# Performance work log

Hardware: AMD Instinct MI355X
Metric: run time of the kernel (lower is better)

Reference implementation:

```python
import jax, jax.numpy as jnp
import numpy as np

B, T, E, H = 2, 2048, 768, 12
D = E // H  # head_dim = 64
EPS = 1e-5


def layer_norm(x, scale, shift):
    mean = x.mean(axis=-1, keepdims=True)
    # torch .var() default is unbiased (ddof=1)
    var = x.var(axis=-1, keepdims=True, ddof=1)
    return scale * (x - mean) / jnp.sqrt(var + EPS) + shift


def gelu(x):
    c = jnp.sqrt(jnp.asarray(2.0 / jnp.pi, dtype=x.dtype))
    return 0.5 * x * (1.0 + jnp.tanh(c * (x + 0.044715 * x * x * x)))


def setup_inputs() -> dict:
    key = jax.random.key(0)
    ks = jax.random.split(key, 12)
    s = 0.02
    return {
        "x": jax.random.normal(ks[0], (B, T, E), jnp.float32),
        "wq": jax.random.normal(ks[1], (E, E), jnp.float32) * s,
        "wk": jax.random.normal(ks[2], (E, E), jnp.float32) * s,
        "wv": jax.random.normal(ks[3], (E, E), jnp.float32) * s,
        "wo": jax.random.normal(ks[4], (E, E), jnp.float32) * s,
        "bo": jnp.zeros((E,), jnp.float32),
        "ln1_scale": jnp.ones((E,), jnp.float32),
        "ln1_shift": jnp.zeros((E,), jnp.float32),
        "ln2_scale": jnp.ones((E,), jnp.float32),
        "ln2_shift": jnp.zeros((E,), jnp.float32),
        "w1": jax.random.normal(ks[5], (E, 4 * E), jnp.float32) * s,
        "b1": jnp.zeros((4 * E,), jnp.float32),
        "w2": jax.random.normal(ks[6], (4 * E, E), jnp.float32) * s,
        "b2": jnp.zeros((E,), jnp.float32),
    }


def reference(x, wq, wk, wv, wo, bo, ln1_scale, ln1_shift, ln2_scale, ln2_shift,
              w1, b1, w2, b2):
    b, t, e = x.shape
    resid = x
    h = layer_norm(x, ln1_scale, ln1_shift)
    # qkv projections (no bias), split heads -> [b, H, t, D]
    q = (h @ wq).reshape(b, t, H, D).transpose(0, 2, 1, 3)
    k = (h @ wk).reshape(b, t, H, D).transpose(0, 2, 1, 3)
    v = (h @ wv).reshape(b, t, H, D).transpose(0, 2, 1, 3)
    scores = jnp.einsum("bhqd,bhkd->bhqk", q, k) / jnp.sqrt(jnp.asarray(D, x.dtype))
    causal = jnp.tril(jnp.ones((t, t), bool))
    scores = jnp.where(causal[None, None], scores, -jnp.inf)
    attn = jax.nn.softmax(scores, axis=-1)  # dropout p=0 (eval)
    ctx = jnp.einsum("bhqk,bhkd->bhqd", attn, v)
    ctx = ctx.transpose(0, 2, 1, 3).reshape(b, t, e)
    h = ctx @ wo + bo
    x = h + resid

    resid = x
    h = layer_norm(x, ln2_scale, ln2_shift)
    h = gelu(h @ w1 + b1) @ w2 + b2
    return h + resid
```

## Files before the change

kernel.cpp:

```cpp
#include <hip/hip_runtime.h>
#include <hip/hip_bf16.h>
#include <math.h>

typedef __bf16 bf16_t;
typedef __bf16 bf16x4 __attribute__((ext_vector_type(4)));
typedef __bf16 bf16x8 __attribute__((ext_vector_type(8)));
typedef float f32x4 __attribute__((ext_vector_type(4)));

#define TB 2048
#define BB 2
#define EE 768
#define HH 12
#define MM (BB * TB)
#define E3 (3 * EE)
#define E4 (4 * EE)

#define GLL16(g, l)                                                        \
  __builtin_amdgcn_global_load_lds(                                       \
      (const __attribute__((address_space(1))) void*)(g),                 \
      (__attribute__((address_space(3))) void*)(l), 16, 0, 0)

__global__ __launch_bounds__(256) void k_transpose_all(
    const float* __restrict__ wq, const float* __restrict__ wk,
    const float* __restrict__ wv, const float* __restrict__ wo,
    const float* __restrict__ w1, const float* __restrict__ w2,
    bf16_t* __restrict__ wqkvT, bf16_t* __restrict__ woT,
    bf16_t* __restrict__ w1T, bf16_t* __restrict__ w2T) {
  __shared__ bf16_t tile[64][72];
  int id = blockIdx.x;
  const float* src;
  bf16_t* dst;
  int K, N, kt, nt;
  if (id < 576) {
    int m = id / 144, t = id - m * 144;
    kt = (t / 12) * 64; nt = (t % 12) * 64; K = 768; N = 768;
    src = (m == 0) ? wq : (m == 1) ? wk : (m == 2) ? wv : wo;
    dst = (m < 3) ? wqkvT + (size_t)m * 768 * 768 : woT;
  } else if (id < 1152) {
    int t = id - 576;
    kt = (t / 48) * 64; nt = (t % 48) * 64; K = 768; N = 3072;
    src = w1; dst = w1T;
  } else {
    int t = id - 1152;
    kt = (t / 12) * 64; nt = (t % 12) * 64; K = 3072; N = 768;
    src = w2; dst = w2T;
  }
  int tid = threadIdx.x;
  int r = tid >> 2, c = (tid & 3) * 16;
  const float* s = src + (size_t)(kt + r) * N + nt + c;
  bf16x8 t0, t1;
#pragma unroll
  for (int j = 0; j < 8; j++) { t0[j] = (bf16_t)s[j]; t1[j] = (bf16_t)s[8 + j]; }
  *(bf16x8*)&tile[r][c] = t0;
  *(bf16x8*)&tile[r][c + 8] = t1;
  __syncthreads();
  bf16_t* d = dst + (size_t)(nt + r) * K + kt + c;
  bf16x8 o0, o1;
#pragma unroll
  for (int j = 0; j < 8; j++) { o0[j] = tile[c + j][r]; o1[j] = tile[c + 8 + j][r]; }
  *(bf16x8*)d = o0;
  *(bf16x8*)(d + 8) = o1;
}

__global__ __launch_bounds__(256) void k_transpose_v(const bf16_t* __restrict__ qkv,
                                                     bf16_t* __restrict__ vt) {
  __shared__ bf16_t tile[64][72];
  int tt = blockIdx.x;
  int bh = blockIdx.y;
  int b = bh / HH, h = bh - b * HH;
  int tid = threadIdx.x;
  int r = tid >> 2, c = (tid & 3) * 16;
  const bf16_t* src = qkv + (size_t)(b * TB + tt * 64 + r) * E3 + 2 * EE + h * 64 + c;
  *(bf16x8*)&tile[r][c] = *(const bf16x8*)src;
  *(bf16x8*)&tile[r][c + 8] = *(const bf16x8*)(src + 8);
  __syncthreads();
  bf16_t* dst = vt + ((size_t)bh * 64 + r) * TB + tt * 64 + c;
  bf16x8 o0, o1;
#pragma unroll
  for (int j = 0; j < 8; j++) { o0[j] = tile[c + j][r]; o1[j] = tile[c + 8 + j][r]; }
  *(bf16x8*)dst = o0;
  *(bf16x8*)(dst + 8) = o1;
}

__global__ __launch_bounds__(256) void k_layernorm_bf16(
    const float* __restrict__ x, const float* __restrict__ sc,
    const float* __restrict__ sh, bf16_t* __restrict__ out) {
  int wave = threadIdx.x >> 6, lane = threadIdx.x & 63;
  int row = blockIdx.x * 4 + wave;
  const float* xr = x + (size_t)row * EE;
  float v[12];
  float s = 0.f, sq = 0.f;
#pragma unroll
  for (int i = 0; i < 12; i++) {
    float t = xr[lane + 64 * i];
    v[i] = t; s += t; sq += t * t;
  }
#pragma unroll
  for (int off = 1; off < 64; off <<= 1) {
    s += __shfl_xor(s, off);
    sq += __shfl_xor(sq, off);
  }
  float mean = s * (1.f / EE);
  float var = (sq - (float)EE * mean * mean) * (1.f / (EE - 1));
  float rstd = rsqrtf(var + 1e-5f);
  bf16_t* orow = out + (size_t)row * EE;
#pragma unroll
  for (int i = 0; i < 12; i++) {
    int e = lane + 64 * i;
    orow[e] = (bf16_t)(sc[e] * (v[i] - mean) * rstd + sh[e]);
  }
}

__global__ __launch_bounds__(256) void k_gemm128(
    const bf16_t* __restrict__ A, const bf16_t* __restrict__ Bt,
    int M, int N, int K, int kLen, int epi,
    float* __restrict__ outf, bf16_t* __restrict__ outb,
    const float* __restrict__ bias, const float* __restrict__ resid) {
  __shared__ bf16_t As[128 * 64];
  __shared__ bf16_t Bs[128 * 64];
  int tid = threadIdx.x;
  int wave = tid >> 6, lane = tid & 63;
  int m0 = blockIdx.y * 128, n0 = blockIdx.x * 128;
  int kOff = blockIdx.z * kLen;
  int wm = (wave >> 1) * 64, wn = (wave & 1) * 64;
  int lm = lane & 15, quad = lane >> 4;

  int srow = wave * 32 + (lane >> 3);
  int scol = (((lane & 7) ^ ((lane >> 3) & 7)) * 8);
  const bf16_t* Ap = A + (size_t)(m0 + srow) * K + kOff + scol;
  const bf16_t* Bp = Bt + (size_t)(n0 + srow) * K + kOff + scol;
  bf16_t* ldsA[4];
  bf16_t* ldsB[4];
#pragma unroll
  for (int j = 0; j < 4; j++) {
    ldsA[j] = &As[(wave * 32 + j * 8) * 64];
    ldsB[j] = &Bs[(wave * 32 + j * 8) * 64];
  }

  f32x4 acc[4][4];
#pragma unroll
  for (int i = 0; i < 4; i++)
#pragma unroll
    for (int j = 0; j < 4; j++) acc[i][j] = (f32x4){0.f, 0.f, 0.f, 0.f};

  for (int k0 = 0; k0 < kLen; k0 += 64) {
    __syncthreads();
#pragma unroll
    for (int j = 0; j < 4; j++) {
      GLL16(Ap + k0 + (size_t)j * 8 * K, ldsA[j]);
      GLL16(Bp + k0 + (size_t)j * 8 * K, ldsB[j]);
    }
    __syncthreads();
#pragma unroll
    for (int c = 0; c < 2; c++) {
      bf16x8 af[4], bfr[4];
#pragma unroll
      for (int i = 0; i < 4; i++) {
        int r = wm + i * 16 + lm;
        af[i] = *(const bf16x8*)&As[r * 64 + (((c * 4 + quad) ^ (lm & 7)) * 8)];
      }
#pragma unroll
      for (int j = 0; j < 4; j++) {
        int r = wn + j * 16 + lm;
        bfr[j] = *(const bf16x8*)&Bs[r * 64 + (((c * 4 + quad) ^ (lm & 7)) * 8)];
      }
#pragma unroll
      for (int i = 0; i < 4; i++)
#pragma unroll
        for (int j = 0; j < 4; j++)
          acc[i][j] = __builtin_amdgcn_mfma_f32_16x16x32_bf16(af[i], bfr[j], acc[i][j], 0, 0, 0);
    }
  }

  size_t pbase = (size_t)blockIdx.z * M * N;
#pragma unroll
  for (int i = 0; i < 4; i++) {
#pragma unroll
    for (int j = 0; j < 4; j++) {
      int col = n0 + wn + j * 16 + lm;
#pragma unroll
      for (int r = 0; r < 4; r++) {
        int row = m0 + wm + i * 16 + quad * 4 + r;
        size_t o = (size_t)row * N + col;
        float c = acc[i][j][r];
        if (epi == 0) {
          outb[o] = (bf16_t)c;
        } else if (epi == 1) {
          float xg = c + bias[col];
          float u2 = xg * 1.5957691216057308f + xg * xg * xg * 0.07135481627561393f;
          float t = 1.f - 2.f / (__expf(u2) + 1.f);
          outb[o] = (bf16_t)(0.5f * xg * (1.f + t));
        } else if (epi == 2) {
          outf[o] = c + bias[col] + resid[o];
        } else {
          outb[pbase + o] = (bf16_t)c;
        }
      }
    }
  }
}

__global__ __launch_bounds__(256) void k_reduce_ln2(
    const bf16_t* __restrict__ p, const float* __restrict__ bo_,
    const float* __restrict__ x, const float* __restrict__ sc,
    const float* __restrict__ sh, float* __restrict__ x1,
    bf16_t* __restrict__ h2) {
  int wave = threadIdx.x >> 6, lane = threadIdx.x & 63;
  int row = blockIdx.x * 4 + wave;
  const bf16_t* p0 = p + (size_t)row * EE;
  const bf16_t* p1 = p + (size_t)(MM + row) * EE;
  const float* xr = x + (size_t)row * EE;
  float v[12];
  float s = 0.f, sq = 0.f;
#pragma unroll
  for (int i = 0; i < 12; i++) {
    int e = lane + 64 * i;
    float t = (float)p0[e] + (float)p1[e] + bo_[e] + xr[e];
    v[i] = t; s += t; sq += t * t;
  }
#pragma unroll
  for (int off = 1; off < 64; off <<= 1) {
    s += __shfl_xor(s, off);
    sq += __shfl_xor(sq, off);
  }
  float mean = s * (1.f / EE);
  float var = (sq - (float)EE * mean * mean) * (1.f / (EE - 1));
  float rstd = rsqrtf(var + 1e-5f);
  float* x1r = x1 + (size_t)row * EE;
  bf16_t* h2r = h2 + (size_t)row * EE;
#pragma unroll
  for (int i = 0; i < 12; i++) {
    int e = lane + 64 * i;
    x1r[e] = v[i];
    h2r[e] = (bf16_t)(sc[e] * (v[i] - mean) * rstd + sh[e]);
  }
}

__global__ __launch_bounds__(256) void k_reduce_out(
    const bf16_t* __restrict__ p, const float* __restrict__ b2,
    const float* __restrict__ x1, float* __restrict__ out) {
  size_t e = ((size_t)blockIdx.x * 256 + threadIdx.x) * 8;
  bf16x8 a0 = *(const bf16x8*)(p + e);
  bf16x8 a1 = *(const bf16x8*)(p + (size_t)MM * EE + e);
  bf16x8 a2 = *(const bf16x8*)(p + (size_t)2 * MM * EE + e);
  bf16x8 a3 = *(const bf16x8*)(p + (size_t)3 * MM * EE + e);
  int col = (int)(e % EE);
#pragma unroll
  for (int j = 0; j < 8; j++) {
    out[e + j] = (float)a0[j] + (float)a1[j] + (float)a2[j] + (float)a3[j] +
                 b2[col + j] + x1[e + j];
  }
}

__global__ __launch_bounds__(256) void k_attn_mfma(const bf16_t* __restrict__ qkv,
                                                   const bf16_t* __restrict__ vt,
                                                   bf16_t* __restrict__ opart,
                                                   float* __restrict__ lpart) {
  __shared__ bf16_t Qs[64][72];
  __shared__ bf16_t Ks[64][72];
  __shared__ bf16_t Vt[64][72];
  __shared__ bf16_t Ps[4][16][72];

  int bh = blockIdx.x;
  int y = blockIdx.y;
  int qt, c, nsplit;
  if (y < 32)      { qt = 24 + (y >> 2); c = y & 3; nsplit = 4; }
  else if (y < 56) { int z = y - 32; qt = 16 + z / 3; c = z - (z / 3) * 3; nsplit = 3; }
  else if (y < 72) { int z = y - 56; qt = 8 + (z >> 1); c = z & 1; nsplit = 2; }
  else             { qt = y - 72; c = 0; nsplit = 1; }
  int ntiles = qt + 1;
  int len = (ntiles + nsplit - 1) / nsplit;
  int k0t = c * len;
  int k1t = k0t + len < ntiles ? k0t + len : ntiles;

  int b = bh / HH, h = bh - b * HH;
  int q0 = qt * 64;
  int tid = threadIdx.x;
  int wave = tid >> 6, lane = tid & 63;
  int lm = lane & 15, quad = lane >> 4;
  int sr = tid >> 2, sc = (tid & 3) * 16;
  const bf16_t* vt_bh = vt + (size_t)bh * 64 * TB;

  {
    const bf16_t* src = qkv + (size_t)(b * TB + q0 + sr) * E3 + h * 64 + sc;
    bf16x8 u0 = *(const bf16x8*)src;
    bf16x8 u1 = *(const bf16x8*)(src + 8);
    bf16x8 s0, s1;
#pragma unroll
    for (int j = 0; j < 8; j++) {
      s0[j] = (bf16_t)((float)u0[j] * 0.125f);
      s1[j] = (bf16_t)((float)u1[j] * 0.125f);
    }
    *(bf16x8*)(&Qs[sr][sc]) = s0;
    *(bf16x8*)(&Qs[sr][sc + 8]) = s1;
  }
  __syncthreads();
  bf16x8 qf0 = *(const bf16x8*)(&Qs[wave * 16 + lm][quad * 8]);
  bf16x8 qf1 = *(const bf16x8*)(&Qs[wave * 16 + lm][32 + quad * 8]);

  f32x4 o_acc[4];
#pragma unroll
  for (int nt = 0; nt < 4; nt++) o_acc[nt] = (f32x4){0.f, 0.f, 0.f, 0.f};
  float l = 0.f;

  for (int kt = k0t; kt < k1t; kt++) {
    __syncthreads();
    {
      const bf16_t* ksrc = qkv + (size_t)(b * TB + kt * 64 + sr) * E3 + EE + h * 64 + sc;
      *(bf16x8*)(&Ks[sr][sc]) = *(const bf16x8*)ksrc;
      *(bf16x8*)(&Ks[sr][sc + 8]) = *(const bf16x8*)(ksrc + 8);
      const bf16_t* vsrc = vt_bh + (size_t)sr * TB + kt * 64 + sc;
      *(bf16x8*)(&Vt[sr][sc]) = *(const bf16x8*)vsrc;
      *(bf16x8*)(&Vt[sr][sc + 8]) = *(const bf16x8*)(vsrc + 8);
    }
    __syncthreads();

    f32x4 st[4];
#pragma unroll
    for (int nt = 0; nt < 4; nt++) {
      st[nt] = (f32x4){0.f, 0.f, 0.f, 0.f};
      bf16x8 kf0 = *(const bf16x8*)(&Ks[nt * 16 + lm][quad * 8]);
      bf16x8 kf1 = *(const bf16x8*)(&Ks[nt * 16 + lm][32 + quad * 8]);
      st[nt] = __builtin_amdgcn_mfma_f32_16x16x32_bf16(kf0, qf0, st[nt], 0, 0, 0);
      st[nt] = __builtin_amdgcn_mfma_f32_16x16x32_bf16(kf1, qf1, st[nt], 0, 0, 0);
    }
    if (kt == qt) {
#pragma unroll
      for (int nt = 0; nt < 4; nt++)
#pragma unroll
        for (int r = 0; r < 4; r++)
          if (nt * 16 + quad * 4 + r > wave * 16 + lm) st[nt][r] = -1e30f;
    }

#pragma unroll
    for (int nt = 0; nt < 4; nt++) {
      bf16x4 pk;
#pragma unroll
      for (int r = 0; r < 4; r++) {
        float p = __expf(st[nt][r]);
        pk[r] = (bf16_t)p;
        l += p;
      }
      *(bf16x4*)(&Ps[wave][lm][nt * 16 + quad * 4]) = pk;
    }

    bf16x8 pf0 = *(const bf16x8*)(&Ps[wave][lm][quad * 8]);
    bf16x8 pf1 = *(const bf16x8*)(&Ps[wave][lm][32 + quad * 8]);
#pragma unroll
    for (int nt = 0; nt < 4; nt++) {
      bf16x8 vf0 = *(const bf16x8*)(&Vt[nt * 16 + lm][quad * 8]);
      bf16x8 vf1 = *(const bf16x8*)(&Vt[nt * 16 + lm][32 + quad * 8]);
      o_acc[nt] = __builtin_amdgcn_mfma_f32_16x16x32_bf16(pf0, vf0, o_acc[nt], 0, 0, 0);
      o_acc[nt] = __builtin_amdgcn_mfma_f32_16x16x32_bf16(pf1, vf1, o_acc[nt], 0, 0, 0);
    }
  }

  l += __shfl_xor(l, 16);
  l += __shfl_xor(l, 32);
  size_t slot = (size_t)(bh * 32 + qt) * 4 + c;
  if (quad == 0) lpart[slot * 64 + wave * 16 + lm] = l;
  bf16_t* ob = opart + slot * 4096;
#pragma unroll
  for (int nt = 0; nt < 4; nt++)
#pragma unroll
    for (int r = 0; r < 4; r++)
      ob[(wave * 16 + quad * 4 + r) * 64 + nt * 16 + lm] = (bf16_t)o_acc[nt][r];
}

__global__ __launch_bounds__(256) void k_attn_reduce(
    const bf16_t* __restrict__ opart, const float* __restrict__ lpart,
    bf16_t* __restrict__ ctx) {
  int bh = blockIdx.x, qt = blockIdx.y;
  int b = bh / HH, h = bh - b * HH;
  int nsplit = qt >= 24 ? 4 : qt >= 16 ? 3 : qt >= 8 ? 2 : 1;
  int tid = threadIdx.x;
  int q = tid >> 2, dc = (tid & 3) * 16;
  size_t slot0 = (size_t)(bh * 32 + qt) * 4;
  float o[16];
#pragma unroll
  for (int j = 0; j < 16; j++) o[j] = 0.f;
  float lsum = 0.f;
  for (int c = 0; c < nsplit; c++) {
    const bf16_t* p = opart + (slot0 + c) * 4096 + q * 64 + dc;
    bf16x8 u0 = *(const bf16x8*)p;
    bf16x8 u1 = *(const bf16x8*)(p + 8);
#pragma unroll
    for (int j = 0; j < 8; j++) { o[j] += (float)u0[j]; o[8 + j] += (float)u1[j]; }
    lsum += lpart[(slot0 + c) * 64 + q];
  }
  float inv = 1.f / lsum;
  bf16_t* dst = ctx + (size_t)(b * TB + qt * 64 + q) * EE + h * 64 + dc;
  bf16x8 d0, d1;
#pragma unroll
  for (int j = 0; j < 8; j++) { d0[j] = (bf16_t)(o[j] * inv); d1[j] = (bf16_t)(o[8 + j] * inv); }
  *(bf16x8*)dst = d0;
  *(bf16x8*)(dst + 8) = d1;
}

extern "C" void kernel_launch(void* const* d_in, const int* in_sizes, int n_in,
                              void* d_out, int out_size, void* d_ws, size_t ws_size,
                              hipStream_t stream) {
  const float* x    = (const float*)d_in[0];
  const float* wq   = (const float*)d_in[1];
  const float* wk   = (const float*)d_in[2];
  const float* wv   = (const float*)d_in[3];
  const float* wo   = (const float*)d_in[4];
  const float* bo   = (const float*)d_in[5];
  const float* ln1s = (const float*)d_in[6];
  const float* ln1b = (const float*)d_in[7];
  const float* ln2s = (const float*)d_in[8];
  const float* ln2b = (const float*)d_in[9];
  const float* w1   = (const float*)d_in[10];
  const float* b1   = (const float*)d_in[11];
  const float* w2   = (const float*)d_in[12];
  const float* b2   = (const float*)d_in[13];
  float* out = (float*)d_out;

  char* ws = (char*)d_ws;
  size_t off = 0;
  auto alloc = [&](size_t bytes) {
    char* p = ws + off;
    off += (bytes + 255) & ~(size_t)255;
    return p;
  };
  float*  x1    = (float*) alloc((size_t)MM * EE * 4);
  bf16_t* w1T   = (bf16_t*)alloc((size_t)E4 * EE * 2);
  bf16_t* w2T   = (bf16_t*)alloc((size_t)EE * E4 * 2);
  bf16_t* woT   = (bf16_t*)alloc((size_t)EE * EE * 2);
  bf16_t* wqkvT = (bf16_t*)alloc((size_t)E3 * EE * 2);
  bf16_t* hbf   = (bf16_t*)alloc((size_t)MM * EE * 2);
  bf16_t* h2    = (bf16_t*)alloc((size_t)MM * EE * 2);
  bf16_t* vtb   = (bf16_t*)alloc((size_t)BB * HH * 64 * TB * 2);
  bf16_t* part  = (bf16_t*)alloc((size_t)4 * MM * EE * 2);
  bf16_t* opart = (bf16_t*)alloc((size_t)BB * HH * 32 * 4 * 4096 * 2);
  float*  lpart = (float*) alloc((size_t)BB * HH * 32 * 4 * 64 * 4);
  bf16_t* qkv   = (bf16_t*)alloc((size_t)MM * E3 * 2);
  bf16_t* hmid  = qkv;

  k_transpose_all<<<1728, 256, 0, stream>>>(wq, wk, wv, wo, w1, w2,
                                            wqkvT, woT, w1T, w2T);
  k_layernorm_bf16<<<MM / 4, 256, 0, stream>>>(x, ln1s, ln1b, hbf);
  k_gemm128<<<dim3(E3 / 128, MM / 128), 256, 0, stream>>>(hbf, wqkvT, MM, E3, EE, EE, 0,
                                                          nullptr, qkv, nullptr, nullptr);
  k_transpose_v<<<dim3(TB / 64, BB * HH), 256, 0, stream>>>(qkv, vtb);
  k_attn_mfma<<<dim3(BB * HH, 80), 256, 0, stream>>>(qkv, vtb, opart, lpart);
  k_attn_reduce<<<dim3(BB * HH, TB / 64), 256, 0, stream>>>(opart, lpart, hbf);
  k_gemm128<<<dim3(EE / 128, MM / 128, 2), 256, 0, stream>>>(hbf, woT, MM, EE, EE, 384, 3,
                                                             nullptr, part, nullptr, nullptr);
  k_reduce_ln2<<<MM / 4, 256, 0, stream>>>(part, bo, x, ln2s, ln2b, x1, h2);
  k_gemm128<<<dim3(E4 / 128, MM / 128), 256, 0, stream>>>(h2, w1T, MM, E4, EE, EE, 1,
                                                          nullptr, hmid, b1, nullptr);
  k_gemm128<<<dim3(EE / 128, MM / 128, 4), 256, 0, stream>>>(hmid, w2T, MM, EE, E4, E4 / 4, 3,
                                                             nullptr, part, nullptr, nullptr);
  k_reduce_out<<<(MM * EE / 8 + 255) / 256, 256, 0, stream>>>(part, b2, x1, out);
}
```

Measured before the change: 288.1 us.

## Double-buffer GEMM LDS tiles with K=32 steps and split-K 4 for out-projection

The 128x128 GEMM now uses two LDS buffers of K=32 and prefetches the next tile with global_load_lds while MFMAs run on the current one. This replaces the two barriers per K=64 step and is meant to overlap global-to-LDS transfer with compute. The XOR swizzle is dropped, which risks LDS bank conflicts on the fragment reads. The out-projection split-K goes from 2 to 4 with the LN2 reduce summing four partials, trading extra partial traffic for more blocks.

```diff
diff --git a/kernel.cpp b/kernel.cpp
--- a/kernel.cpp
+++ b/kernel.cpp
@@ -116,8 +116,8 @@
     int M, int N, int K, int kLen, int epi,
     float* __restrict__ outf, bf16_t* __restrict__ outb,
     const float* __restrict__ bias, const float* __restrict__ resid) {
-  __shared__ bf16_t As[128 * 64];
-  __shared__ bf16_t Bs[128 * 64];
+  __shared__ bf16_t As[2][128 * 32];
+  __shared__ bf16_t Bs[2][128 * 32];
   int tid = threadIdx.x;
   int wave = tid >> 6, lane = tid & 63;
   int m0 = blockIdx.y * 128, n0 = blockIdx.x * 128;
@@ -125,17 +125,12 @@
   int wm = (wave >> 1) * 64, wn = (wave & 1) * 64;
   int lm = lane & 15, quad = lane >> 4;
 
-  int srow = wave * 32 + (lane >> 3);
-  int scol = (((lane & 7) ^ ((lane >> 3) & 7)) * 8);
-  const bf16_t* Ap = A + (size_t)(m0 + srow) * K + kOff + scol;
-  const bf16_t* Bp = Bt + (size_t)(n0 + srow) * K + kOff + scol;
-  bf16_t* ldsA[4];
-  bf16_t* ldsB[4];
-#pragma unroll
-  for (int j = 0; j < 4; j++) {
-    ldsA[j] = &As[(wave * 32 + j * 8) * 64];
-    ldsB[j] = &Bs[(wave * 32 + j * 8) * 64];
-  }
+  int srow = wave * 32 + (lane >> 2);
+  int scol = (lane & 3) * 8;
+  const bf16_t* Ap0 = A + (size_t)(m0 + srow) * K + kOff + scol;
+  const bf16_t* Ap1 = A + (size_t)(m0 + srow + 16) * K + kOff + scol;
+  const bf16_t* Bp0 = Bt + (size_t)(n0 + srow) * K + kOff + scol;
+  const bf16_t* Bp1 = Bt + (size_t)(n0 + srow + 16) * K + kOff + scol;
 
   f32x4 acc[4][4];
 #pragma unroll
@@ -143,33 +138,35 @@
 #pragma unroll
     for (int j = 0; j < 4; j++) acc[i][j] = (f32x4){0.f, 0.f, 0.f, 0.f};
 
-  for (int k0 = 0; k0 < kLen; k0 += 64) {
+  int nIter = kLen >> 5;
+  GLL16(Ap0, &As[0][(wave * 32) * 32]);
+  GLL16(Ap1, &As[0][(wave * 32 + 16) * 32]);
+  GLL16(Bp0, &Bs[0][(wave * 32) * 32]);
+  GLL16(Bp1, &Bs[0][(wave * 32 + 16) * 32]);
+
+  for (int k = 0; k < nIter; k++) {
     __syncthreads();
-#pragma unroll
-    for (int j = 0; j < 4; j++) {
-      GLL16(Ap + k0 + (size_t)j * 8 * K, ldsA[j]);
-      GLL16(Bp + k0 + (size_t)j * 8 * K, ldsB[j]);
-    }
-    __syncthreads();
-#pragma unroll
-    for (int c = 0; c < 2; c++) {
-      bf16x8 af[4], bfr[4];
-#pragma unroll
-      for (int i = 0; i < 4; i++) {
-        int r = wm + i * 16 + lm;
-        af[i] = *(const bf16x8*)&As[r * 64 + (((c * 4 + quad) ^ (lm & 7)) * 8)];
-      }
-#pragma unroll
-      for (int j = 0; j < 4; j++) {
-        int r = wn + j * 16 + lm;
-        bfr[j] = *(const bf16x8*)&Bs[r * 64 + (((c * 4 + quad) ^ (lm & 7)) * 8)];
-      }
-#pragma unroll
-      for (int i = 0; i < 4; i++)
-#pragma unroll
-        for (int j = 0; j < 4; j++)
-          acc[i][j] = __builtin_amdgcn_mfma_f32_16x16x32_bf16(af[i], bfr[j], acc[i][j], 0, 0, 0);
-    }
+    int buf = k & 1;
+    if (k + 1 < nIter) {
+      int nb = buf ^ 1;
+      int ko = (k + 1) << 5;
+      GLL16(Ap0 + ko, &As[nb][(wave * 32) * 32]);
+      GLL16(Ap1 + ko, &As[nb][(wave * 32 + 16) * 32]);
+      GLL16(Bp0 + ko, &Bs[nb][(wave * 32) * 32]);
+      GLL16(Bp1 + ko, &Bs[nb][(wave * 32 + 16) * 32]);
+    }
+    bf16x8 af[4], bfr[4];
+#pragma unroll
+    for (int i = 0; i < 4; i++)
+      af[i] = *(const bf16x8*)&As[buf][(wm + i * 16 + lm) * 32 + quad * 8];
+#pragma unroll
+    for (int j = 0; j < 4; j++)
+      bfr[j] = *(const bf16x8*)&Bs[buf][(wn + j * 16 + lm) * 32 + quad * 8];
+#pragma unroll
+    for (int i = 0; i < 4; i++)
+#pragma unroll
+      for (int j = 0; j < 4; j++)
+        acc[i][j] = __builtin_amdgcn_mfma_f32_16x16x32_bf16(af[i], bfr[j], acc[i][j], 0, 0, 0);
   }
 
   size_t pbase = (size_t)blockIdx.z * M * N;
@@ -208,14 +205,17 @@
   int wave = threadIdx.x >> 6, lane = threadIdx.x & 63;
   int row = blockIdx.x * 4 + wave;
   const bf16_t* p0 = p + (size_t)row * EE;
-  const bf16_t* p1 = p + (size_t)(MM + row) * EE;
+  const bf16_t* p1 = p0 + (size_t)MM * EE;
+  const bf16_t* p2 = p0 + (size_t)2 * MM * EE;
+  const bf16_t* p3 = p0 + (size_t)3 * MM * EE;
   const float* xr = x + (size_t)row * EE;
   float v[12];
   float s = 0.f, sq = 0.f;
 #pragma unroll
   for (int i = 0; i < 12; i++) {
     int e = lane + 64 * i;
-    float t = (float)p0[e] + (float)p1[e] + bo_[e] + xr[e];
+    float t = (float)p0[e] + (float)p1[e] + (float)p2[e] + (float)p3[e] +
+              bo_[e] + xr[e];
     v[i] = t; s += t; sq += t * t;
   }
 #pragma unroll
@@ -445,7 +445,7 @@
   k_transpose_v<<<dim3(TB / 64, BB * HH), 256, 0, stream>>>(qkv, vtb);
   k_attn_mfma<<<dim3(BB * HH, 80), 256, 0, stream>>>(qkv, vtb, opart, lpart);
   k_attn_reduce<<<dim3(BB * HH, TB / 64), 256, 0, stream>>>(opart, lpart, hbf);
-  k_gemm128<<<dim3(EE / 128, MM / 128, 2), 256, 0, stream>>>(hbf, woT, MM, EE, EE, 384, 3,
+  k_gemm128<<<dim3(EE / 128, MM / 128, 4), 256, 0, stream>>>(hbf, woT, MM, EE, EE, 192, 3,
                                                              nullptr, part, nullptr, nullptr);
   k_reduce_ln2<<<MM / 4, 256, 0, stream>>>(part, bo, x, ln2s, ln2b, x1, h2);
   k_gemm128<<<dim3(E4 / 128, MM / 128), 256, 0, stream>>>(h2, w1T, MM, E4, EE, EE, 1,
```

After: 300.5 us. +4.3%, slower.

## Fuse LN1 into weight prep, write V transposed from QKV GEMM, prescale Wq

Applied to the files above, without the earlier changes.

Merges the LayerNorm-1 kernel into the weight transpose/convert kernel as extra blocks, removing one launch. The QKV GEMM epilogue now writes V tiles directly in transposed per-head layout, which removes the separate V transpose kernel and its read/write pass. The 1/sqrt(D) scale is folded into Wq during conversion, so the attention kernel loads Q without rescaling. This changes bf16 rounding of Q slightly, and the transposed V stores are 4-element strided writes.

```diff
diff --git a/kernel.cpp b/kernel.cpp
--- a/kernel.cpp
+++ b/kernel.cpp
@@ -20,22 +20,54 @@
       (const __attribute__((address_space(1))) void*)(g),                 \
       (__attribute__((address_space(3))) void*)(l), 16, 0, 0)
 
-__global__ __launch_bounds__(256) void k_transpose_all(
+__global__ __launch_bounds__(256) void k_prep(
     const float* __restrict__ wq, const float* __restrict__ wk,
     const float* __restrict__ wv, const float* __restrict__ wo,
     const float* __restrict__ w1, const float* __restrict__ w2,
     bf16_t* __restrict__ wqkvT, bf16_t* __restrict__ woT,
-    bf16_t* __restrict__ w1T, bf16_t* __restrict__ w2T) {
+    bf16_t* __restrict__ w1T, bf16_t* __restrict__ w2T,
+    const float* __restrict__ x, const float* __restrict__ ln1s,
+    const float* __restrict__ ln1b, bf16_t* __restrict__ hbf) {
   __shared__ bf16_t tile[64][72];
   int id = blockIdx.x;
+  int tid = threadIdx.x;
+  if (id >= 1728) {
+    int wave = tid >> 6, lane = tid & 63;
+    int row = (id - 1728) * 4 + wave;
+    const float* xr = x + (size_t)row * EE;
+    float v[12];
+    float s = 0.f, sq = 0.f;
+#pragma unroll
+    for (int i = 0; i < 12; i++) {
+      float t = xr[lane + 64 * i];
+      v[i] = t; s += t; sq += t * t;
+    }
+#pragma unroll
+    for (int off = 1; off < 64; off <<= 1) {
+      s += __shfl_xor(s, off);
+      sq += __shfl_xor(sq, off);
+    }
+    float mean = s * (1.f / EE);
+    float var = (sq - (float)EE * mean * mean) * (1.f / (EE - 1));
+    float rstd = rsqrtf(var + 1e-5f);
+    bf16_t* orow = hbf + (size_t)row * EE;
+#pragma unroll
+    for (int i = 0; i < 12; i++) {
+      int e = lane + 64 * i;
+      orow[e] = (bf16_t)(ln1s[e] * (v[i] - mean) * rstd + ln1b[e]);
+    }
+    return;
+  }
   const float* src;
   bf16_t* dst;
   int K, N, kt, nt;
+  float scl = 1.f;
   if (id < 576) {
     int m = id / 144, t = id - m * 144;
     kt = (t / 12) * 64; nt = (t % 12) * 64; K = 768; N = 768;
     src = (m == 0) ? wq : (m == 1) ? wk : (m == 2) ? wv : wo;
     dst = (m < 3) ? wqkvT + (size_t)m * 768 * 768 : woT;
+    if (m == 0) scl = 0.125f;
   } else if (id < 1152) {
     int t = id - 576;
     kt = (t / 48) * 64; nt = (t % 48) * 64; K = 768; N = 3072;
@@ -45,12 +77,14 @@
     kt = (t / 12) * 64; nt = (t % 12) * 64; K = 3072; N = 768;
     src = w2; dst = w2T;
   }
-  int tid = threadIdx.x;
   int r = tid >> 2, c = (tid & 3) * 16;
   const float* s = src + (size_t)(kt + r) * N + nt + c;
   bf16x8 t0, t1;
 #pragma unroll
-  for (int j = 0; j < 8; j++) { t0[j] = (bf16_t)s[j]; t1[j] = (bf16_t)s[8 + j]; }
+  for (int j = 0; j < 8; j++) {
+    t0[j] = (bf16_t)(s[j] * scl);
+    t1[j] = (bf16_t)(s[8 + j] * scl);
+  }
   *(bf16x8*)&tile[r][c] = t0;
   *(bf16x8*)&tile[r][c + 8] = t1;
   __syncthreads();
@@ -62,60 +96,12 @@
   *(bf16x8*)(d + 8) = o1;
 }
 
-__global__ __launch_bounds__(256) void k_transpose_v(const bf16_t* __restrict__ qkv,
-                                                     bf16_t* __restrict__ vt) {
-  __shared__ bf16_t tile[64][72];
-  int tt = blockIdx.x;
-  int bh = blockIdx.y;
-  int b = bh / HH, h = bh - b * HH;
-  int tid = threadIdx.x;
-  int r = tid >> 2, c = (tid & 3) * 16;
-  const bf16_t* src = qkv + (size_t)(b * TB + tt * 64 + r) * E3 + 2 * EE + h * 64 + c;
-  *(bf16x8*)&tile[r][c] = *(const bf16x8*)src;
-  *(bf16x8*)&tile[r][c + 8] = *(const bf16x8*)(src + 8);
-  __syncthreads();
-  bf16_t* dst = vt + ((size_t)bh * 64 + r) * TB + tt * 64 + c;
-  bf16x8 o0, o1;
-#pragma unroll
-  for (int j = 0; j < 8; j++) { o0[j] = tile[c + j][r]; o1[j] = tile[c + 8 + j][r]; }
-  *(bf16x8*)dst = o0;
-  *(bf16x8*)(dst + 8) = o1;
-}
-
-__global__ __launch_bounds__(256) void k_layernorm_bf16(
-    const float* __restrict__ x, const float* __restrict__ sc,
-    const float* __restrict__ sh, bf16_t* __restrict__ out) {
-  int wave = threadIdx.x >> 6, lane = threadIdx.x & 63;
-  int row = blockIdx.x * 4 + wave;
-  const float* xr = x + (size_t)row * EE;
-  float v[12];
-  float s = 0.f, sq = 0.f;
-#pragma unroll
-  for (int i = 0; i < 12; i++) {
-    float t = xr[lane + 64 * i];
-    v[i] = t; s += t; sq += t * t;
-  }
-#pragma unroll
-  for (int off = 1; off < 64; off <<= 1) {
-    s += __shfl_xor(s, off);
-    sq += __shfl_xor(sq, off);
-  }
-  float mean = s * (1.f / EE);
-  float var = (sq - (float)EE * mean * mean) * (1.f / (EE - 1));
-  float rstd = rsqrtf(var + 1e-5f);
-  bf16_t* orow = out + (size_t)row * EE;
-#pragma unroll
-  for (int i = 0; i < 12; i++) {
-    int e = lane + 64 * i;
-    orow[e] = (bf16_t)(sc[e] * (v[i] - mean) * rstd + sh[e]);
-  }
-}
-
 __global__ __launch_bounds__(256) void k_gemm128(
     const bf16_t* __restrict__ A, const bf16_t* __restrict__ Bt,
     int M, int N, int K, int kLen, int epi,
     float* __restrict__ outf, bf16_t* __restrict__ outb,
-    const float* __restrict__ bias, const float* __restrict__ resid) {
+    const float* __restrict__ bias, const float* __restrict__ resid,
+    bf16_t* __restrict__ vtout) {
   __shared__ bf16_t As[128 * 64];
   __shared__ bf16_t Bs[128 * 64];
   int tid = threadIdx.x;
@@ -173,11 +159,22 @@
   }
 
   size_t pbase = (size_t)blockIdx.z * M * N;
+  bool vtile = (epi == 0) && (n0 >= 2 * EE);
 #pragma unroll
   for (int i = 0; i < 4; i++) {
 #pragma unroll
     for (int j = 0; j < 4; j++) {
       int col = n0 + wn + j * 16 + lm;
+      if (vtile) {
+        int hv = (col - 2 * EE) >> 6, d = (col - 2 * EE) & 63;
+        int row0 = m0 + wm + i * 16 + quad * 4;
+        int bb = row0 >> 11, t0 = row0 & (TB - 1);
+        bf16x4 v4;
+#pragma unroll
+        for (int r = 0; r < 4; r++) v4[r] = (bf16_t)acc[i][j][r];
+        *(bf16x4*)&vtout[((size_t)(bb * HH + hv) * 64 + d) * TB + t0] = v4;
+        continue;
+      }
 #pragma unroll
       for (int r = 0; r < 4; r++) {
         int row = m0 + wm + i * 16 + quad * 4 + r;
@@ -208,7 +205,7 @@
   int wave = threadIdx.x >> 6, lane = threadIdx.x & 63;
   int row = blockIdx.x * 4 + wave;
   const bf16_t* p0 = p + (size_t)row * EE;
-  const bf16_t* p1 = p + (size_t)(MM + row) * EE;
+  const bf16_t* p1 = p0 + (size_t)MM * EE;
   const float* xr = x + (size_t)row * EE;
   float v[12];
   float s = 0.f, sq = 0.f;
@@ -283,16 +280,8 @@
 
   {
     const bf16_t* src = qkv + (size_t)(b * TB + q0 + sr) * E3 + h * 64 + sc;
-    bf16x8 u0 = *(const bf16x8*)src;
-    bf16x8 u1 = *(const bf16x8*)(src + 8);
-    bf16x8 s0, s1;
-#pragma unroll
-    for (int j = 0; j < 8; j++) {
-      s0[j] = (bf16_t)((float)u0[j] * 0.125f);
-      s1[j] = (bf16_t)((float)u1[j] * 0.125f);
-    }
-    *(bf16x8*)(&Qs[sr][sc]) = s0;
-    *(bf16x8*)(&Qs[sr][sc + 8]) = s1;
+    *(bf16x8*)(&Qs[sr][sc]) = *(const bf16x8*)src;
+    *(bf16x8*)(&Qs[sr][sc + 8]) = *(const bf16x8*)(src + 8);
   }
   __syncthreads();
   bf16x8 qf0 = *(const bf16x8*)(&Qs[wave * 16 + lm][quad * 8]);
@@ -437,20 +426,18 @@
   bf16_t* qkv   = (bf16_t*)alloc((size_t)MM * E3 * 2);
   bf16_t* hmid  = qkv;
 
-  k_transpose_all<<<1728, 256, 0, stream>>>(wq, wk, wv, wo, w1, w2,
-                                            wqkvT, woT, w1T, w2T);
-  k_layernorm_bf16<<<MM / 4, 256, 0, stream>>>(x, ln1s, ln1b, hbf);
+  k_prep<<<2752, 256, 0, stream>>>(wq, wk, wv, wo, w1, w2,
+                                   wqkvT, woT, w1T, w2T, x, ln1s, ln1b, hbf);
   k_gemm128<<<dim3(E3 / 128, MM / 128), 256, 0, stream>>>(hbf, wqkvT, MM, E3, EE, EE, 0,
-                                                          nullptr, qkv, nullptr, nullptr);
-  k_transpose_v<<<dim3(TB / 64, BB * HH), 256, 0, stream>>>(qkv, vtb);
+                                                          nullptr, qkv, nullptr, nullptr, vtb);
   k_attn_mfma<<<dim3(BB * HH, 80), 256, 0, stream>>>(qkv, vtb, opart, lpart);
   k_attn_reduce<<<dim3(BB * HH, TB / 64), 256, 0, stream>>>(opart, lpart, hbf);
   k_gemm128<<<dim3(EE / 128, MM / 128, 2), 256, 0, stream>>>(hbf, woT, MM, EE, EE, 384, 3,
-                                                             nullptr, part, nullptr, nullptr);
+                                                             nullptr, part, nullptr, nullptr, nullptr);
   k_reduce_ln2<<<MM / 4, 256, 0, stream>>>(part, bo, x, ln2s, ln2b, x1, h2);
   k_gemm128<<<dim3(E4 / 128, MM / 128), 256, 0, stream>>>(h2, w1T, MM, E4, EE, EE, 1,
-                                                          nullptr, hmid, b1, nullptr);
+                                                          nullptr, hmid, b1, nullptr, nullptr);
   k_gemm128<<<dim3(EE / 128, MM / 128, 4), 256, 0, stream>>>(hmid, w2T, MM, EE, E4, E4 / 4, 3,
-                                                             nullptr, part, nullptr, nullptr);
+                                                             nullptr, part, nullptr, nullptr, nullptr);
   k_reduce_out<<<(MM * EE / 8 + 255) / 256, 256, 0, stream>>>(part, b2, x1, out);
 }
```

Measured after the change: 285.4 us. About the same (-0.9%).
